# Optimization experiments

Hardware: AMD Instinct MI355X
Metric: run time of the kernel (lower is better)

## Reference

```python
import jax, jax.numpy as jnp
import numpy as np

HEADS = 8
GROUP_SIZE = 256
DIM = 512
QK_DIM = 512
M_GLOBAL = 64


def setup_inputs() -> dict:
    key = jax.random.key(0)
    ks = jax.random.split(key, 9)
    B, N = 2, 16384
    normed_x = jax.random.normal(ks[0], (B, N, DIM), dtype=jnp.float32)
    # idx_last must be a per-batch permutation of [0, N): gather reorders tokens,
    # the final scatter puts them back.
    perm = jnp.stack([jax.random.permutation(jax.random.fold_in(ks[1], b), N) for b in range(B)])
    idx_last = perm[..., None].astype(jnp.int32)  # [B, N, 1]
    dq = QK_DIM // HEADS
    dv = DIM // HEADS
    k_global = jax.random.normal(ks[2], (HEADS, M_GLOBAL, dq), dtype=jnp.float32)
    v_global = jax.random.normal(ks[3], (HEADS, M_GLOBAL, dv), dtype=jnp.float32)
    s = 0.02
    Wq = jax.random.normal(ks[4], (DIM, QK_DIM), dtype=jnp.float32) * s
    Wk = jax.random.normal(ks[5], (DIM, QK_DIM), dtype=jnp.float32) * s
    Wv = jax.random.normal(ks[6], (DIM, DIM), dtype=jnp.float32) * s
    Wproj = jax.random.normal(ks[7], (DIM, DIM), dtype=jnp.float32) * s
    return {"normed_x": normed_x, "idx_last": idx_last, "k_global": k_global,
            "v_global": v_global, "Wq": Wq, "Wk": Wk, "Wv": Wv, "Wproj": Wproj}


def _iasa_forward(normed_x, idx_last, k_global, v_global, Wq, Wk, Wv, Wproj):
    B, N, dim = normed_x.shape
    H = HEADS
    gs = min(N, GROUP_SIZE)
    ng = -(-N // gs)
    pad_n = ng * gs - N
    q = normed_x @ Wq  # [B, N, qk]
    k = normed_x @ Wk  # [B, N, qk]
    v = normed_x @ Wv  # [B, N, dim]
    # gather-reorder tokens
    q = jnp.take_along_axis(q, jnp.broadcast_to(idx_last, q.shape), axis=1)
    k = jnp.take_along_axis(k, jnp.broadcast_to(idx_last, k.shape), axis=1)
    v = jnp.take_along_axis(v, jnp.broadcast_to(idx_last, v.shape), axis=1)
    # pad queries with flipped tail to [B, ng*gs, qk]
    pq = jnp.concatenate([q, q[:, N - pad_n:N][:, ::-1]], axis=1)
    # pad k/v with flipped last (pad_n+gs) tokens -> length (ng+1)*gs
    pk = jnp.concatenate([k, k[:, N - pad_n - gs:N][:, ::-1]], axis=1)
    pv = jnp.concatenate([v, v[:, N - pad_n - gs:N][:, ::-1]], axis=1)
    dq = pq.shape[-1] // H
    dv = dim // H
    # queries: [B, ng, H, gs, dq]
    qg = pq.reshape(B, ng, gs, H, dq).transpose(0, 1, 3, 2, 4)
    # overlapping windows of size 2*gs, stride gs (unfold equivalent)
    kgrp = pk.reshape(B, ng + 1, gs, H, dq)
    vgrp = pv.reshape(B, ng + 1, gs, H, dv)
    kwin = jnp.concatenate([kgrp[:, :-1], kgrp[:, 1:]], axis=2).transpose(0, 1, 3, 2, 4)  # [B,ng,H,2gs,dq]
    vwin = jnp.concatenate([vgrp[:, :-1], vgrp[:, 1:]], axis=2).transpose(0, 1, 3, 2, 4)  # [B,ng,H,2gs,dv]
    scale = 1.0 / jnp.sqrt(jnp.asarray(dq, dtype=qg.dtype))
    # local attention
    s1 = jnp.einsum('bghqd,bghkd->bghqk', qg, kwin) * scale
    out1 = jnp.einsum('bghqk,bghkd->bghqd', jax.nn.softmax(s1, axis=-1), vwin)
    # global attention (k_global/v_global shared across batch and groups)
    s2 = jnp.einsum('bghqd,hmd->bghqm', qg, k_global) * scale
    out2 = jnp.einsum('bghqm,hmd->bghqd', jax.nn.softmax(s2, axis=-1), v_global)
    out = (out1 + out2).transpose(0, 1, 3, 2, 4).reshape(B, ng * gs, H * dv)[:, :N]
    # scatter back (inverse of the gather, since idx_last is a permutation)
    idxo = jnp.broadcast_to(idx_last, out.shape)
    bi = jnp.arange(B)[:, None, None]
    ci = jnp.arange(H * dv)[None, None, :]
    out = out.at[bi, idxo, ci].set(out)
    return out @ Wproj


def reference(normed_x, idx_last, k_global, v_global, Wq, Wk, Wv, Wproj):
    return _iasa_forward(normed_x, idx_last, k_global, v_global, Wq, Wk, Wv, Wproj)
```

## Files before the change

### kernel.cpp

```cpp
#include <hip/hip_runtime.h>
#include <hip/hip_bf16.h>

#define B_   2
#define N_   16384
#define H_   8
#define GS_  256
#define NG_  64

typedef unsigned short u16;
typedef __attribute__((ext_vector_type(8))) short bf16x8;
typedef __attribute__((ext_vector_type(4))) float f32x4;
typedef __attribute__((ext_vector_type(8))) unsigned short us8;
typedef __attribute__((ext_vector_type(4))) unsigned short us4;
typedef __attribute__((ext_vector_type(4))) unsigned int u32x4;
typedef __attribute__((ext_vector_type(2))) unsigned int u32x2;

__device__ __forceinline__ u16 f2b(float f){
  union { float f; unsigned u; } v; v.f = f;
  unsigned r = v.u + 0x7fffu + ((v.u >> 16) & 1u);
  return (u16)(r >> 16);
}

__device__ __forceinline__ u16 f2bh(float f){
  __hip_bfloat16 h = __float2bfloat16(f);
  u16 u; __builtin_memcpy(&u, &h, 2);
  return u;
}

__device__ __forceinline__ unsigned pk2(float a, float b){
  unsigned r;
  asm("v_cvt_pk_bf16_f32 %0, %1, %2" : "=v"(r) : "v"(a), "v"(b));
  return r;
}

__device__ __forceinline__ void gload16(const void* g, const void* lds){
  __builtin_amdgcn_global_load_lds(
      (const __attribute__((address_space(1))) void*)g,
      (__attribute__((address_space(3))) void*)lds, 16, 0, 0);
}

__device__ __forceinline__ bf16x8 lds_read8(const u16* base, int row, int coloff){
  int byte = (row*128 + coloff) ^ ((row & 7) << 4);
  return *(const bf16x8*)((const char*)base + byte);
}

__device__ __forceinline__ void stout(float* p, float v){ *p = v; }
__device__ __forceinline__ void stout(u16* p, float v){ *p = f2b(v); }

__global__ void cvt_f32_bf16(const float4* __restrict__ in, us4* __restrict__ out, int n4){
  int i = blockIdx.x * 256 + threadIdx.x;
  if (i < n4){
    float4 v = in[i];
    us4 o;
    o[0] = f2b(v.x); o[1] = f2b(v.y); o[2] = f2b(v.z); o[3] = f2b(v.w);
    out[i] = o;
  }
}

__global__ void cvt_kv(const float4* __restrict__ kg, const float4* __restrict__ vg,
                       us4* __restrict__ ok, us4* __restrict__ ov){
  int i = blockIdx.x * 256 + threadIdx.x;
  const float4* in = blockIdx.y ? vg : kg;
  us4* out = blockIdx.y ? ov : ok;
  float4 v = in[i];
  us4 o;
  o[0] = f2b(v.x); o[1] = f2b(v.y); o[2] = f2b(v.z); o[3] = f2b(v.w);
  out[i] = o;
}

__global__ void cvt_w_t(const float* __restrict__ W0, const float* __restrict__ W1,
                        const float* __restrict__ W2, const float* __restrict__ W3,
                        u16* __restrict__ T0, u16* __restrict__ T1,
                        u16* __restrict__ T2, u16* __restrict__ T3)
{
  int z = blockIdx.z;
  const float* W = (z==0)?W0:((z==1)?W1:((z==2)?W2:W3));
  u16* T = (z==0)?T0:((z==1)?T1:((z==2)?T2:T3));
  __shared__ float tile[16][17];
  int tx = threadIdx.x & 15, ty = threadIdx.x >> 4;
  int k0 = blockIdx.x*16, n0 = blockIdx.y*16;
  tile[ty][tx] = W[(k0+ty)*512 + n0 + tx];
  __syncthreads();
  T[(n0+ty)*512 + k0 + tx] = f2b(tile[tx][ty]);
}

template<typename OUT_T, bool MULTI, bool GATHA, bool SCATC>
__global__ __launch_bounds__(256, 2) void gemm_bf16k(
    const u16* __restrict__ A,
    const u16* __restrict__ Wt0, const u16* __restrict__ Wt1, const u16* __restrict__ Wt2,
    const int* __restrict__ perm,
    OUT_T* __restrict__ C, int ldc)
{
  __shared__ u16 Al[128*64];
  __shared__ u16 Bl[128*64];
  const int tid = threadIdx.x;
  const int l = tid & 63, w = tid >> 6;
  const int lr = l & 15, lg = l >> 4;
  const int bm = blockIdx.y, bn = blockIdx.x;
  const int wr = (w >> 1) * 64, wc = (w & 1) * 64;

  const u16* Wt; int ocolb; float qsc;
  if (MULTI){
    int wsel = bn >> 2;
    Wt = (wsel == 0) ? Wt0 : ((wsel == 1) ? Wt1 : Wt2);
    ocolb = (bn & 3) * 128;
    qsc = (wsel == 0) ? 0.18033688f : 1.0f;
  } else { Wt = Wt0; ocolb = bn * 128; qsc = 1.0f; }

  int arows[4];
#pragma unroll
  for (int i = 0; i < 4; ++i){
    int r = bm*128 + i*32 + (tid >> 3);
    arows[i] = GATHA ? ((r & ~(N_-1)) + perm[r]) : r;
  }

  f32x4 acc[4][4];
#pragma unroll
  for (int m = 0; m < 4; ++m)
#pragma unroll
    for (int n = 0; n < 4; ++n) acc[m][n] = (f32x4){0.f,0.f,0.f,0.f};

  const int c8 = tid & 7;
  for (int kk = 0; kk < 512; kk += 64){
#pragma unroll
    for (int i = 0; i < 4; ++i){
      int o = i*4096 + tid*16;
      int brow = o >> 7;
      gload16(A  + (size_t)arows[i]*512 + kk + c8*8, (const char*)Al + i*4096 + w*1024);
      gload16(Wt + (size_t)(ocolb + brow)*512 + kk + c8*8, (const char*)Bl + i*4096 + w*1024);
    }
    __syncthreads();
#pragma unroll
    for (int ks = 0; ks < 2; ++ks){
      bf16x8 af[4], bfv[4];
#pragma unroll
      for (int m = 0; m < 4; ++m) af[m]  = *(const bf16x8*)&Al[(wr + m*16 + lr)*64 + ks*32 + lg*8];
#pragma unroll
      for (int n = 0; n < 4; ++n) bfv[n] = *(const bf16x8*)&Bl[(wc + n*16 + lr)*64 + ks*32 + lg*8];
#pragma unroll
      for (int m = 0; m < 4; ++m)
#pragma unroll
        for (int n = 0; n < 4; ++n)
          acc[m][n] = __builtin_amdgcn_mfma_f32_16x16x32_bf16(af[m], bfv[n], acc[m][n], 0, 0, 0);
    }
    __syncthreads();
  }
#pragma unroll
  for (int m = 0; m < 4; ++m)
#pragma unroll
    for (int n = 0; n < 4; ++n)
#pragma unroll
      for (int j = 0; j < 4; ++j){
        int row = bm*128 + wr + m*16 + lg*4 + j;
        int col = bn*128 + wc + n*16 + lr;
        size_t orow = SCATC ? (size_t)((row & ~(N_-1)) + perm[row]) : (size_t)row;
        stout(&C[orow*ldc + col], acc[m][n][j] * qsc);
      }
}

#define COMPUTE_CHUNK(KBUF, VBUF, ACC, LAC) do { \
  f32x4 s_[4][4]; \
  _Pragma("unroll") \
  for (int n_ = 0; n_ < 4; ++n_){ _Pragma("unroll") for (int m_ = 0; m_ < 4; ++m_) s_[n_][m_] = (f32x4){0.f,0.f,0.f,0.f}; } \
  _Pragma("unroll") \
  for (int ks_ = 0; ks_ < 2; ++ks_){ \
    bf16x8 kf_[4]; \
    _Pragma("unroll") for (int n_ = 0; n_ < 4; ++n_) kf_[n_] = lds_read8((KBUF), n_*16 + lr, ks_*64 + lg*16); \
    _Pragma("unroll") for (int n_ = 0; n_ < 4; ++n_){ \
      _Pragma("unroll") for (int m_ = 0; m_ < 4; ++m_) \
        s_[n_][m_] = __builtin_amdgcn_mfma_f32_16x16x32_bf16(kf_[n_], qf[m_][ks_], s_[n_][m_], 0, 0, 0); } } \
  _Pragma("unroll") \
  for (int m_ = 0; m_ < 4; ++m_){ \
    float rs_ = 0.f; \
    _Pragma("unroll") for (int n_ = 0; n_ < 4; ++n_){ \
      _Pragma("unroll") for (int j_ = 0; j_ < 4; ++j_){ \
        float p_ = exp2f(s_[n_][m_][j_]); s_[n_][m_][j_] = p_; rs_ += p_; } } \
    (LAC)[m_] += rs_; } \
  _Pragma("unroll") \
  for (int mh_ = 0; mh_ < 2; ++mh_){ \
    _Pragma("unroll") for (int m2_ = 0; m2_ < 2; ++m2_){ \
      int m_ = mh_*2 + m2_; \
      int q_ = m2_*16 + lr; \
      _Pragma("unroll") for (int n_ = 0; n_ < 4; ++n_){ \
        u32x2 pk_; \
        pk_[0] = pk2(s_[n_][m_][0], s_[n_][m_][1]); \
        pk_[1] = pk2(s_[n_][m_][2], s_[n_][m_][3]); \
        int byte_ = (q_*128 + n_*32 + lg*8) ^ ((q_ & 7) << 4); \
        *(u32x2*)((char*)Pw + byte_) = pk_; } } \
    _Pragma("unroll") for (int ks_ = 0; ks_ < 2; ++ks_){ \
      bf16x8 pa_[2], vb_[4]; \
      _Pragma("unroll") for (int m2_ = 0; m2_ < 2; ++m2_) pa_[m2_] = lds_read8(Pw, m2_*16 + lr, ks_*64 + lg*16); \
      _Pragma("unroll") for (int n_ = 0; n_ < 4; ++n_) vb_[n_] = lds_read8((VBUF), n_*16 + lr, ks_*64 + lg*16); \
      _Pragma("unroll") for (int m2_ = 0; m2_ < 2; ++m2_){ \
        _Pragma("unroll") for (int n_ = 0; n_ < 4; ++n_) \
          (ACC)[mh_*2+m2_][n_] = __builtin_amdgcn_mfma_f32_16x16x32_bf16(pa_[m2_], vb_[n_], (ACC)[mh_*2+m2_][n_], 0, 0, 0); } } \
  } \
} while(0)

#define LOADKV(c) do { int c_ = (c); \
  if (c_ < 8){ \
    int p0k_ = g*GS_ + c_*64 + krow_; \
    int p1k_ = p0k_ + 32; \
    int rk0_ = (p0k_ < N_) ? p0k_ : (2*N_ - 1 - p0k_); \
    int rk1_ = (p1k_ < N_) ? p1k_ : (2*N_ - 1 - p1k_); \
    kr0 = *(const us8*)(qkv + (size_t)(b*N_ + rk0_)*1536 + 512 + h*64 + kc8_*8); \
    kr1 = *(const us8*)(qkv + (size_t)(b*N_ + rk1_)*1536 + 512 + h*64 + kc8_*8); \
    int p0v_ = g*GS_ + c_*64 + 2*pair; \
    int p1v_ = p0v_ + 1; \
    int rv0_ = (p0v_ < N_) ? p0v_ : (2*N_ - 1 - p0v_); \
    int rv1_ = (p1v_ < N_) ? p1v_ : (2*N_ - 1 - p1v_); \
    vr0 = *(const us8*)(qkv + (size_t)(b*N_ + rv0_)*1536 + 1024 + h*64 + dvb*8); \
    vr1 = *(const us8*)(qkv + (size_t)(b*N_ + rv1_)*1536 + 1024 + h*64 + dvb*8); \
  } else { \
    kr0 = *(const us8*)(kgb + (size_t)(h*64 + krow_)*64 + kc8_*8); \
    kr1 = *(const us8*)(kgb + (size_t)(h*64 + 32 + krow_)*64 + kc8_*8); \
    vr0 = *(const us8*)(vgb + (size_t)(h*64 + 2*pair)*64 + dvb*8); \
    vr1 = *(const us8*)(vgb + (size_t)(h*64 + 2*pair + 1)*64 + dvb*8); \
  } } while(0)

#define WRITEKV() do { \
  { int r0_ = krow_, r1_ = 32 + krow_; \
    *(us8*)((char*)Kb + ((r0_*128 + kc8_*16) ^ ((r0_ & 7) << 4))) = kr0; \
    *(us8*)((char*)Kb + ((r1_*128 + kc8_*16) ^ ((r1_ & 7) << 4))) = kr1; } \
  _Pragma("unroll") \
  for (int j_ = 0; j_ < 8; ++j_){ \
    int r_ = dvb*8 + j_; \
    int byte_ = (r_*128 + pair*4) ^ ((r_ & 7) << 4); \
    *(unsigned*)((char*)Vb + byte_) = (unsigned)vr0[j_] | ((unsigned)vr1[j_] << 16); } \
} while(0)

__global__ __launch_bounds__(256, 2) void attn_kernel(
    const u16* __restrict__ qkv,
    const u16* __restrict__ kgb,
    const u16* __restrict__ vgb,
    u16* __restrict__ outp)
{
  __shared__ u16 Pl[4][32*64];
  __shared__ u16 Kb[64*64];
  __shared__ u16 Vb[64*64];

  const int tid = threadIdx.x;
  const int l = tid & 63, w = tid >> 6;
  const int lr = l & 15, lg = l >> 4;
  const int pair = tid & 31, dvb = tid >> 5;
  const int krow_ = tid >> 3, kc8_ = tid & 7;

  const int g = blockIdx.x, h = blockIdx.y, b = blockIdx.z;

  bf16x8 qf[4][2];
#pragma unroll
  for (int m = 0; m < 4; ++m){
    int grow = g*GS_ + w*64 + m*16 + lr;
    const u16* qrow = qkv + (size_t)(b*N_ + grow)*1536 + h*64;
#pragma unroll
    for (int ks = 0; ks < 2; ++ks)
      qf[m][ks] = *(const bf16x8*)(qrow + ks*32 + lg*8);
  }

  u16* Pw = Pl[w];

  us8 kr0, kr1, vr0, vr1;
  LOADKV(0);
  WRITEKV();
  __syncthreads();

  f32x4 oacc[4][4];
  float lrun[4];
#pragma unroll
  for (int m = 0; m < 4; ++m)
#pragma unroll
    for (int n = 0; n < 4; ++n) oacc[m][n] = (f32x4){0.f,0.f,0.f,0.f};
#pragma unroll
  for (int m = 0; m < 4; ++m) lrun[m] = 0.f;

  for (int c = 0; c < 8; ++c){
    LOADKV(c + 1);
    COMPUTE_CHUNK(Kb, Vb, oacc, lrun);
    __syncthreads();
    WRITEKV();
    __syncthreads();
  }

  float i1[4];
#pragma unroll
  for (int m = 0; m < 4; ++m){
    float s1 = lrun[m];
    s1 += __shfl_xor(s1, 16); s1 += __shfl_xor(s1, 32);
    i1[m] = 1.f / s1;
  }
#pragma unroll
  for (int m = 0; m < 4; ++m)
#pragma unroll
    for (int j = 0; j < 4; ++j){
      float invb = __shfl(i1[m], lg*4 + j);
#pragma unroll
      for (int n = 0; n < 4; ++n) oacc[m][n][j] *= invb;
    }

  {
    f32x4 s_[4][4];
#pragma unroll
    for (int n_ = 0; n_ < 4; ++n_)
#pragma unroll
      for (int m_ = 0; m_ < 4; ++m_) s_[n_][m_] = (f32x4){0.f,0.f,0.f,0.f};
#pragma unroll
    for (int ks_ = 0; ks_ < 2; ++ks_){
      bf16x8 kf_[4];
#pragma unroll
      for (int n_ = 0; n_ < 4; ++n_) kf_[n_] = lds_read8(Kb, n_*16 + lr, ks_*64 + lg*16);
#pragma unroll
      for (int n_ = 0; n_ < 4; ++n_)
#pragma unroll
        for (int m_ = 0; m_ < 4; ++m_)
          s_[n_][m_] = __builtin_amdgcn_mfma_f32_16x16x32_bf16(kf_[n_], qf[m_][ks_], s_[n_][m_], 0, 0, 0);
    }
#pragma unroll
    for (int m_ = 0; m_ < 4; ++m_){
      float rs_ = 0.f;
#pragma unroll
      for (int n_ = 0; n_ < 4; ++n_)
#pragma unroll
        for (int j_ = 0; j_ < 4; ++j_){
          float p_ = exp2f(s_[n_][m_][j_]); s_[n_][m_][j_] = p_; rs_ += p_;
        }
      rs_ += __shfl_xor(rs_, 16); rs_ += __shfl_xor(rs_, 32);
      float iv_ = 1.f / rs_;
#pragma unroll
      for (int n_ = 0; n_ < 4; ++n_)
#pragma unroll
        for (int j_ = 0; j_ < 4; ++j_) s_[n_][m_][j_] *= iv_;
    }
#pragma unroll
    for (int mh_ = 0; mh_ < 2; ++mh_){
#pragma unroll
      for (int m2_ = 0; m2_ < 2; ++m2_){
        int m_ = mh_*2 + m2_;
        int q_ = m2_*16 + lr;
#pragma unroll
        for (int n_ = 0; n_ < 4; ++n_){
          u32x2 pk_;
          pk_[0] = pk2(s_[n_][m_][0], s_[n_][m_][1]);
          pk_[1] = pk2(s_[n_][m_][2], s_[n_][m_][3]);
          int byte_ = (q_*128 + n_*32 + lg*8) ^ ((q_ & 7) << 4);
          *(u32x2*)((char*)Pw + byte_) = pk_;
        }
      }
#pragma unroll
      for (int ks_ = 0; ks_ < 2; ++ks_){
        bf16x8 pa_[2], vb_[4];
#pragma unroll
        for (int m2_ = 0; m2_ < 2; ++m2_) pa_[m2_] = lds_read8(Pw, m2_*16 + lr, ks_*64 + lg*16);
#pragma unroll
        for (int n_ = 0; n_ < 4; ++n_) vb_[n_] = lds_read8(Vb, n_*16 + lr, ks_*64 + lg*16);
#pragma unroll
        for (int m2_ = 0; m2_ < 2; ++m2_)
#pragma unroll
          for (int n_ = 0; n_ < 4; ++n_)
            oacc[mh_*2+m2_][n_] = __builtin_amdgcn_mfma_f32_16x16x32_bf16(pa_[m2_], vb_[n_], oacc[mh_*2+m2_][n_], 0, 0, 0);
      }
    }
  }

#pragma unroll
  for (int mh = 0; mh < 2; ++mh){
#pragma unroll
    for (int m2 = 0; m2 < 2; ++m2)
#pragma unroll
      for (int n = 0; n < 4; ++n)
#pragma unroll
        for (int j = 0; j < 4; ++j){
          int row = m2*16 + lg*4 + j, col = n*16 + lr;
          int byte = (row*128 + col*2) ^ ((row & 7) << 4);
          *(u16*)((char*)Pw + byte) = f2bh(oacc[mh*2+m2][n][j]);
        }
    __builtin_amdgcn_s_waitcnt(0);
#pragma unroll
    for (int i4 = 0; i4 < 4; ++i4){
      int o = i4*1024 + l*16;
      int row = o >> 7, c8 = (o & 127) >> 4;
      int addr = o ^ ((row & 7) << 4);
      u32x4 d = *(const u32x4*)((const char*)Pw + addr);
      int orow = g*GS_ + w*64 + mh*32 + row;
      *(u32x4*)(outp + (size_t)(b*N_ + orow)*512 + h*64 + c8*8) = d;
    }
  }
}

extern "C" void kernel_launch(void* const* d_in, const int* in_sizes, int n_in,
                              void* d_out, int out_size, void* d_ws, size_t ws_size,
                              hipStream_t stream)
{
  const float* x  = (const float*)d_in[0];
  const int*  idx = (const int*)d_in[1];
  const float* kg = (const float*)d_in[2];
  const float* vg = (const float*)d_in[3];
  const float* Wq = (const float*)d_in[4];
  const float* Wk = (const float*)d_in[5];
  const float* Wv = (const float*)d_in[6];
  const float* Wp = (const float*)d_in[7];
  float* out = (float*)d_out;

  char* ws = (char*)d_ws;
  u16* Xb   = (u16*)ws;
  u16* qkv  = (u16*)(ws + 33554432);
  u16* Wqt  = (u16*)(ws + 134217728);
  u16* Wkt  = (u16*)(ws + 134217728 + 524288);
  u16* Wvt  = (u16*)(ws + 134217728 + 2*524288);
  u16* Wpt  = (u16*)(ws + 134217728 + 3*524288);
  u16* kgb  = (u16*)(ws + 134217728 + 4*524288);
  u16* vgb  = (u16*)(ws + 134217728 + 4*524288 + 65536);
  u16* attn_o = Xb;

  cvt_f32_bf16<<<16384, 256, 0, stream>>>((const float4*)x, (us4*)Xb, 16777216/4);
  cvt_kv<<<dim3(32,2), 256, 0, stream>>>((const float4*)kg, (const float4*)vg,
                                         (us4*)kgb, (us4*)vgb);
  cvt_w_t<<<dim3(32,32,4), 256, 0, stream>>>(Wq, Wk, Wv, Wp, Wqt, Wkt, Wvt, Wpt);
  gemm_bf16k<u16, true, true, false><<<dim3(12,256), 256, 0, stream>>>(Xb, Wqt, Wkt, Wvt, idx, qkv, 1536);
  attn_kernel<<<dim3(64,8,2), 256, 0, stream>>>(qkv, kgb, vgb, attn_o);
  gemm_bf16k<float, false, false, true><<<dim3(4,256), 256, 0, stream>>>(attn_o, Wpt, Wpt, Wpt, idx, out, 512);
}
```

Measured before the change: 207.0 us.

## Shrink score tiles to cut register pressure and raise occupancy to three blocks

The local-attention chunk now computes QK^T scores in 2x2 sub-tiles per (mh, nh) slice and writes them to the P buffer right away, instead of holding a full 4x4 block of score accumulators live. The global-attention block becomes a two-pass softmax: it computes the scores and row sums first, then recomputes the scores and exponentials to write normalized probabilities. Launch bounds rise from 2 to 3 blocks per CU, so the compiler must fit the kernel into fewer VGPRs for more occupancy. The cost is duplicated MFMA and exp work in the global pass, plus a risk of spills if registers still do not fit.

```diff
diff --git a/kernel.cpp b/kernel.cpp
--- a/kernel.cpp
+++ b/kernel.cpp
@@ -159,34 +159,34 @@
 }
 
 #define COMPUTE_CHUNK(KBUF, VBUF, ACC, LAC) do { \
-  f32x4 s_[4][4]; \
-  _Pragma("unroll") \
-  for (int n_ = 0; n_ < 4; ++n_){ _Pragma("unroll") for (int m_ = 0; m_ < 4; ++m_) s_[n_][m_] = (f32x4){0.f,0.f,0.f,0.f}; } \
-  _Pragma("unroll") \
-  for (int ks_ = 0; ks_ < 2; ++ks_){ \
-    bf16x8 kf_[4]; \
-    _Pragma("unroll") for (int n_ = 0; n_ < 4; ++n_) kf_[n_] = lds_read8((KBUF), n_*16 + lr, ks_*64 + lg*16); \
-    _Pragma("unroll") for (int n_ = 0; n_ < 4; ++n_){ \
-      _Pragma("unroll") for (int m_ = 0; m_ < 4; ++m_) \
-        s_[n_][m_] = __builtin_amdgcn_mfma_f32_16x16x32_bf16(kf_[n_], qf[m_][ks_], s_[n_][m_], 0, 0, 0); } } \
-  _Pragma("unroll") \
-  for (int m_ = 0; m_ < 4; ++m_){ \
-    float rs_ = 0.f; \
-    _Pragma("unroll") for (int n_ = 0; n_ < 4; ++n_){ \
-      _Pragma("unroll") for (int j_ = 0; j_ < 4; ++j_){ \
-        float p_ = exp2f(s_[n_][m_][j_]); s_[n_][m_][j_] = p_; rs_ += p_; } } \
-    (LAC)[m_] += rs_; } \
   _Pragma("unroll") \
   for (int mh_ = 0; mh_ < 2; ++mh_){ \
-    _Pragma("unroll") for (int m2_ = 0; m2_ < 2; ++m2_){ \
-      int m_ = mh_*2 + m2_; \
-      int q_ = m2_*16 + lr; \
-      _Pragma("unroll") for (int n_ = 0; n_ < 4; ++n_){ \
-        u32x2 pk_; \
-        pk_[0] = pk2(s_[n_][m_][0], s_[n_][m_][1]); \
-        pk_[1] = pk2(s_[n_][m_][2], s_[n_][m_][3]); \
-        int byte_ = (q_*128 + n_*32 + lg*8) ^ ((q_ & 7) << 4); \
-        *(u32x2*)((char*)Pw + byte_) = pk_; } } \
+    _Pragma("unroll") \
+    for (int nh_ = 0; nh_ < 2; ++nh_){ \
+      f32x4 s_[2][2]; \
+      _Pragma("unroll") for (int n2_ = 0; n2_ < 2; ++n2_){ \
+        _Pragma("unroll") for (int m2_ = 0; m2_ < 2; ++m2_) s_[n2_][m2_] = (f32x4){0.f,0.f,0.f,0.f}; } \
+      _Pragma("unroll") for (int ks_ = 0; ks_ < 2; ++ks_){ \
+        bf16x8 kf_[2]; \
+        _Pragma("unroll") for (int n2_ = 0; n2_ < 2; ++n2_) \
+          kf_[n2_] = lds_read8((KBUF), (nh_*2+n2_)*16 + lr, ks_*64 + lg*16); \
+        _Pragma("unroll") for (int n2_ = 0; n2_ < 2; ++n2_){ \
+          _Pragma("unroll") for (int m2_ = 0; m2_ < 2; ++m2_) \
+            s_[n2_][m2_] = __builtin_amdgcn_mfma_f32_16x16x32_bf16(kf_[n2_], qf[mh_*2+m2_][ks_], s_[n2_][m2_], 0, 0, 0); } } \
+      _Pragma("unroll") for (int m2_ = 0; m2_ < 2; ++m2_){ \
+        float rs_ = 0.f; \
+        int q_ = m2_*16 + lr; \
+        _Pragma("unroll") for (int n2_ = 0; n2_ < 2; ++n2_){ \
+          _Pragma("unroll") for (int j_ = 0; j_ < 4; ++j_){ \
+            float p_ = exp2f(s_[n2_][m2_][j_]); s_[n2_][m2_][j_] = p_; rs_ += p_; } } \
+        (LAC)[mh_*2+m2_] += rs_; \
+        _Pragma("unroll") for (int n2_ = 0; n2_ < 2; ++n2_){ \
+          u32x2 pk_; \
+          pk_[0] = pk2(s_[n2_][m2_][0], s_[n2_][m2_][1]); \
+          pk_[1] = pk2(s_[n2_][m2_][2], s_[n2_][m2_][3]); \
+          int byte_ = (q_*128 + (nh_*2+n2_)*32 + lg*8) ^ ((q_ & 7) << 4); \
+          *(u32x2*)((char*)Pw + byte_) = pk_; } } \
+    } \
     _Pragma("unroll") for (int ks_ = 0; ks_ < 2; ++ks_){ \
       bf16x8 pa_[2], vb_[4]; \
       _Pragma("unroll") for (int m2_ = 0; m2_ < 2; ++m2_) pa_[m2_] = lds_read8(Pw, m2_*16 + lr, ks_*64 + lg*16); \
@@ -229,7 +229,7 @@
     *(unsigned*)((char*)Vb + byte_) = (unsigned)vr0[j_] | ((unsigned)vr1[j_] << 16); } \
 } while(0)
 
-__global__ __launch_bounds__(256, 2) void attn_kernel(
+__global__ __launch_bounds__(256, 3) void attn_kernel(
     const u16* __restrict__ qkv,
     const u16* __restrict__ kgb,
     const u16* __restrict__ vgb,
@@ -298,51 +298,75 @@
     }
 
   {
-    f32x4 s_[4][4];
-#pragma unroll
-    for (int n_ = 0; n_ < 4; ++n_)
-#pragma unroll
-      for (int m_ = 0; m_ < 4; ++m_) s_[n_][m_] = (f32x4){0.f,0.f,0.f,0.f};
-#pragma unroll
-    for (int ks_ = 0; ks_ < 2; ++ks_){
-      bf16x8 kf_[4];
-#pragma unroll
-      for (int n_ = 0; n_ < 4; ++n_) kf_[n_] = lds_read8(Kb, n_*16 + lr, ks_*64 + lg*16);
-#pragma unroll
-      for (int n_ = 0; n_ < 4; ++n_)
-#pragma unroll
-        for (int m_ = 0; m_ < 4; ++m_)
-          s_[n_][m_] = __builtin_amdgcn_mfma_f32_16x16x32_bf16(kf_[n_], qf[m_][ks_], s_[n_][m_], 0, 0, 0);
-    }
-#pragma unroll
-    for (int m_ = 0; m_ < 4; ++m_){
-      float rs_ = 0.f;
-#pragma unroll
-      for (int n_ = 0; n_ < 4; ++n_)
-#pragma unroll
-        for (int j_ = 0; j_ < 4; ++j_){
-          float p_ = exp2f(s_[n_][m_][j_]); s_[n_][m_][j_] = p_; rs_ += p_;
+    float rsg[4] = {0.f, 0.f, 0.f, 0.f};
+#pragma unroll
+    for (int mh_ = 0; mh_ < 2; ++mh_)
+#pragma unroll
+      for (int nh_ = 0; nh_ < 2; ++nh_){
+        f32x4 s_[2][2];
+#pragma unroll
+        for (int n2_ = 0; n2_ < 2; ++n2_)
+#pragma unroll
+          for (int m2_ = 0; m2_ < 2; ++m2_) s_[n2_][m2_] = (f32x4){0.f,0.f,0.f,0.f};
+#pragma unroll
+        for (int ks_ = 0; ks_ < 2; ++ks_){
+          bf16x8 kf_[2];
+#pragma unroll
+          for (int n2_ = 0; n2_ < 2; ++n2_)
+            kf_[n2_] = lds_read8(Kb, (nh_*2+n2_)*16 + lr, ks_*64 + lg*16);
+#pragma unroll
+          for (int n2_ = 0; n2_ < 2; ++n2_)
+#pragma unroll
+            for (int m2_ = 0; m2_ < 2; ++m2_)
+              s_[n2_][m2_] = __builtin_amdgcn_mfma_f32_16x16x32_bf16(kf_[n2_], qf[mh_*2+m2_][ks_], s_[n2_][m2_], 0, 0, 0);
         }
-      rs_ += __shfl_xor(rs_, 16); rs_ += __shfl_xor(rs_, 32);
-      float iv_ = 1.f / rs_;
-#pragma unroll
-      for (int n_ = 0; n_ < 4; ++n_)
-#pragma unroll
-        for (int j_ = 0; j_ < 4; ++j_) s_[n_][m_][j_] *= iv_;
+#pragma unroll
+        for (int m2_ = 0; m2_ < 2; ++m2_)
+#pragma unroll
+          for (int n2_ = 0; n2_ < 2; ++n2_)
+#pragma unroll
+            for (int j_ = 0; j_ < 4; ++j_)
+              rsg[mh_*2+m2_] += exp2f(s_[n2_][m2_][j_]);
+      }
+#pragma unroll
+    for (int m = 0; m < 4; ++m){
+      float s2 = rsg[m];
+      s2 += __shfl_xor(s2, 16); s2 += __shfl_xor(s2, 32);
+      rsg[m] = 1.f / s2;
     }
 #pragma unroll
     for (int mh_ = 0; mh_ < 2; ++mh_){
 #pragma unroll
-      for (int m2_ = 0; m2_ < 2; ++m2_){
-        int m_ = mh_*2 + m2_;
-        int q_ = m2_*16 + lr;
-#pragma unroll
-        for (int n_ = 0; n_ < 4; ++n_){
-          u32x2 pk_;
-          pk_[0] = pk2(s_[n_][m_][0], s_[n_][m_][1]);
-          pk_[1] = pk2(s_[n_][m_][2], s_[n_][m_][3]);
-          int byte_ = (q_*128 + n_*32 + lg*8) ^ ((q_ & 7) << 4);
-          *(u32x2*)((char*)Pw + byte_) = pk_;
+      for (int nh_ = 0; nh_ < 2; ++nh_){
+        f32x4 s_[2][2];
+#pragma unroll
+        for (int n2_ = 0; n2_ < 2; ++n2_)
+#pragma unroll
+          for (int m2_ = 0; m2_ < 2; ++m2_) s_[n2_][m2_] = (f32x4){0.f,0.f,0.f,0.f};
+#pragma unroll
+        for (int ks_ = 0; ks_ < 2; ++ks_){
+          bf16x8 kf_[2];
+#pragma unroll
+          for (int n2_ = 0; n2_ < 2; ++n2_)
+            kf_[n2_] = lds_read8(Kb, (nh_*2+n2_)*16 + lr, ks_*64 + lg*16);
+#pragma unroll
+          for (int n2_ = 0; n2_ < 2; ++n2_)
+#pragma unroll
+            for (int m2_ = 0; m2_ < 2; ++m2_)
+              s_[n2_][m2_] = __builtin_amdgcn_mfma_f32_16x16x32_bf16(kf_[n2_], qf[mh_*2+m2_][ks_], s_[n2_][m2_], 0, 0, 0);
+        }
+#pragma unroll
+        for (int m2_ = 0; m2_ < 2; ++m2_){
+          float iv_ = rsg[mh_*2+m2_];
+          int q_ = m2_*16 + lr;
+#pragma unroll
+          for (int n2_ = 0; n2_ < 2; ++n2_){
+            u32x2 pk_;
+            pk_[0] = pk2(exp2f(s_[n2_][m2_][0])*iv_, exp2f(s_[n2_][m2_][1])*iv_);
+            pk_[1] = pk2(exp2f(s_[n2_][m2_][2])*iv_, exp2f(s_[n2_][m2_][3])*iv_);
+            int byte_ = (q_*128 + (nh_*2+n2_)*32 + lg*8) ^ ((q_ & 7) << 4);
+            *(u32x2*)((char*)Pw + byte_) = pk_;
+          }
         }
       }
 #pragma unroll
```

New measurement: 311.7 us. +50.6%, slower.
